# Kernel optimization log

Measured on AMD Instinct MI355X. Metric: run time of the kernel, lower is better.

## Reference

```python
import jax, jax.numpy as jnp
import numpy as np

N = 8192          # total nodes in the batch of graphs
ATOM = 64         # atom_feats
HID = 128         # hidden_feats
HEADS = 8         # num_heads
NUM_GRAPHS = 256  # number of graphs (max value of `batch`)
NEG_SLOPE = 0.2   # LeakyReLU slope in GAT attention


def setup_inputs() -> dict:
    key = jax.random.key(0)
    ks = jax.random.split(key, 16)
    x = jax.random.normal(ks[0], (N, ATOM), dtype=jnp.float32)
    adj = (jax.random.uniform(ks[1], (N, N)) < 0.01).astype(jnp.float32)
    adj = jnp.maximum(adj, jnp.eye(N, dtype=jnp.float32))
    batch = jnp.sort(jax.random.randint(ks[2], (N,), 0, NUM_GRAPHS)).astype(jnp.int32)

    def u(k, shape, fan_in):
        lim = 1.0 / np.sqrt(fan_in)
        return jax.random.uniform(k, shape, jnp.float32, -lim, lim)

    in1 = HID * HEADS
    params = dict(
        W0=u(ks[3], (ATOM, HID), ATOM), a0_src=u(ks[4], (HID,), HID), a0_dst=u(ks[5], (HID,), HID),
        W1=u(ks[6], (in1, HID), in1), a1_src=u(ks[7], (HID,), HID), a1_dst=u(ks[8], (HID,), HID),
        W2=u(ks[9], (in1, HID), in1), a2_src=u(ks[10], (HID,), HID), a2_dst=u(ks[11], (HID,), HID),
        fc_w=u(ks[12], (HID, 1), HID), fc_b=u(ks[13], (1,), HID),
    )
    return dict(x=x, adj=adj, batch=batch, **params)


def _gat_layer(h_in, W, a_src, a_dst, mask):
    # standard dense GAT: Wh, e_ij = leakyrelu(a_src.Wh_i + a_dst.Wh_j), masked softmax, aggregate
    h = h_in @ W                                         # [N, HID]
    e = jax.nn.leaky_relu((h @ a_src)[:, None] + (h @ a_dst)[None, :], NEG_SLOPE)  # [N, N]
    e = jnp.where(mask, e, jnp.float32(-1e9))
    attn = jax.nn.softmax(e, axis=1)                     # [N, N]
    return attn @ h                                      # [N, HID]


def reference(x, adj, batch, W0, a0_src, a0_dst, W1, a1_src, a1_dst, W2, a2_src, a2_dst, fc_w, fc_b):
    # eval mode: dropout is identity. The torch module calls the SAME layer instance per head,
    # so concat of heads == tile, and the final stacked mean == a single layer call.
    mask = adj > 0
    h0 = _gat_layer(x, W0, a0_src, a0_dst, mask)
    x1 = jax.nn.relu(jnp.tile(h0, (1, HEADS)))           # [N, HID*HEADS]
    h1 = _gat_layer(x1, W1, a1_src, a1_dst, mask)
    x2 = jax.nn.relu(jnp.tile(h1, (1, HEADS)))
    h2 = _gat_layer(x2, W2, a2_src, a2_dst, mask)        # mean over identical heads == h2
    # global mean pool over graphs
    sums = jax.ops.segment_sum(h2, batch, num_segments=NUM_GRAPHS)           # [G, HID]
    cnt = jax.ops.segment_sum(jnp.ones((N, 1), h2.dtype), batch, num_segments=NUM_GRAPHS)
    pooled = sums / jnp.maximum(cnt, 1.0)
    out = pooled @ fc_w + fc_b                           # [G, 1]
    return out[:, 0]
```

## Files before the change

kernel.cpp:

```cpp
#include <hip/hip_runtime.h>
#include <hip/hip_fp16.h>
#include <cstdint>
#include <cstddef>

#define NN 8192
#define ATOMF 64
#define HID 128
#define HEADS 8
#define NG 256
#define ELLW 192
#define NEGSLOPE 0.2f

typedef unsigned long long u64;

__global__ __launch_bounds__(256, 4) void k_scan_ell(const float* __restrict__ adj,
                                                     int* __restrict__ ell,
                                                     int4* __restrict__ tb) {
    __shared__ u64 bml[4][128];
    int t = threadIdx.x, wid = t >> 6, l = t & 63;
    int row = blockIdx.x * 4 + wid;
    const float4* a4 = (const float4*)(adj + (size_t)row * NN);
    u64* bmr = bml[wid];
    #pragma unroll 8
    for (int s = 0; s < 32; ++s) {
        float4 v = a4[s * 64 + l];
        u64 b0 = __ballot(v.x > 0.f);
        u64 b1 = __ballot(v.y > 0.f);
        u64 b2 = __ballot(v.z > 0.f);
        u64 b3 = __ballot(v.w > 0.f);
        if (l < 4) bmr[s * 4 + l] = (l == 0) ? b0 : (l == 1) ? b1 : (l == 2) ? b2 : b3;
    }
    __syncthreads();
    u64 w0 = bmr[2 * l];
    u64 w1 = bmr[2 * l + 1];
    int c = __popcll(w0) + __popcll(w1);
    int incl = c;
    #pragma unroll
    for (int o = 1; o < 64; o <<= 1) {
        int u = __shfl_up(incl, o);
        if (l >= o) incl += u;
    }
    int pos = incl - c;
    int total = __shfl(incl, 63);
    if (l == 0) {
        int4 b;
        b.x = b.y = b.z = 0;
        b.w = total < ELLW ? total : ELLW;
        tb[row] = b;
    }
    int* er = ell + (size_t)row * ELLW;
    int gw0 = 2 * l, gw1 = 2 * l + 1;
    int base0 = (gw0 >> 2) * 256 + (gw0 & 3);
    int base1 = (gw1 >> 2) * 256 + (gw1 & 3);
    while (w0) {
        int bit = __builtin_ctzll(w0);
        w0 &= w0 - 1;
        if (pos < ELLW) er[pos++] = base0 + 4 * bit;
    }
    while (w1) {
        int bit = __builtin_ctzll(w1);
        w1 &= w1 - 1;
        if (pos < ELLW) er[pos++] = base1 + 4 * bit;
    }
}

__global__ __launch_bounds__(256) void k_front2(
    const float* __restrict__ x,
    const float* __restrict__ W0, const float* __restrict__ a0s, const float* __restrict__ a0d,
    const float* __restrict__ W1, const float* __restrict__ W2,
    float* __restrict__ Wr1, float* __restrict__ Wr2,
    __half* __restrict__ g016, float* __restrict__ ssrc, float* __restrict__ sdst) {
    int b = blockIdx.x, t = threadIdx.x;
    if (b < 128) {
        const float* W = (b < 64) ? W1 : W2;
        float* Wr = (b < 64) ? Wr1 : Wr2;
        int i = (b & 63) * 256 + t;
        int k = i >> 7, cc = i & 127;
        float s = 0.f;
        #pragma unroll
        for (int h = 0; h < HEADS; ++h) s += W[(size_t)(h * HID + k) * HID + cc];
        Wr[i] = s;
    } else {
        __shared__ float Xl[32 * ATOMF];
        int row0 = (b - 128) * 32;
        const float4* Xg = (const float4*)(x + (size_t)row0 * ATOMF);
        float4* Xl4 = (float4*)Xl;
        #pragma unroll
        for (int i = t; i < 32 * ATOMF / 4; i += 256) Xl4[i] = Xg[i];
        __syncthreads();
        int cg = t & 31, rg = t >> 5;
        int c0 = cg * 4;
        float acc[4][4];
        #pragma unroll
        for (int r = 0; r < 4; ++r)
            #pragma unroll
            for (int c = 0; c < 4; ++c) acc[r][c] = 0.f;
        for (int k = 0; k < ATOMF; k += 4) {
            float4 w0 = *(const float4*)(W0 + (size_t)(k + 0) * HID + c0);
            float4 w1 = *(const float4*)(W0 + (size_t)(k + 1) * HID + c0);
            float4 w2 = *(const float4*)(W0 + (size_t)(k + 2) * HID + c0);
            float4 w3 = *(const float4*)(W0 + (size_t)(k + 3) * HID + c0);
            #pragma unroll
            for (int r = 0; r < 4; ++r) {
                float4 xv = *(const float4*)(&Xl[(rg * 4 + r) * ATOMF + k]);
                acc[r][0] += xv.x * w0.x + xv.y * w1.x + xv.z * w2.x + xv.w * w3.x;
                acc[r][1] += xv.x * w0.y + xv.y * w1.y + xv.z * w2.y + xv.w * w3.y;
                acc[r][2] += xv.x * w0.z + xv.y * w1.z + xv.z * w2.z + xv.w * w3.z;
                acc[r][3] += xv.x * w0.w + xv.y * w1.w + xv.z * w2.w + xv.w * w3.w;
            }
        }
        float4 asv = *(const float4*)(a0s + c0);
        float4 adv = *(const float4*)(a0d + c0);
        #pragma unroll
        for (int r = 0; r < 4; ++r) {
            int row = row0 + rg * 4 + r;
            __half2 p0 = __floats2half2_rn(acc[r][0], acc[r][1]);
            __half2 p1 = __floats2half2_rn(acc[r][2], acc[r][3]);
            __half2* gp = (__half2*)(g016 + (size_t)row * HID + c0);
            gp[0] = p0; gp[1] = p1;
            float ps = acc[r][0] * asv.x + acc[r][1] * asv.y + acc[r][2] * asv.z + acc[r][3] * asv.w;
            float pd = acc[r][0] * adv.x + acc[r][1] * adv.y + acc[r][2] * adv.z + acc[r][3] * adv.w;
            #pragma unroll
            for (int o = 16; o; o >>= 1) {
                ps += __shfl_xor(ps, o);
                pd += __shfl_xor(pd, o);
            }
            if (cg == 0) { ssrc[row] = ps; sdst[row] = pd; }
        }
    }
}

template<int DO_GEMM>
__global__ __launch_bounds__(256, 8) void k_layer(
    const __half* __restrict__ h16, const float* __restrict__ ssrc_in,
    const float* __restrict__ sdst_in,
    const int* __restrict__ ell, const int4* __restrict__ tb,
    const float* __restrict__ Wr, const float* __restrict__ as_,
    const float* __restrict__ ad_,
    __half* __restrict__ gout16, float* __restrict__ gout32,
    float* __restrict__ ssrc_out, float* __restrict__ sdst_out) {
    __shared__ float wls[4][ELLW + 4];
    __shared__ int   jls[4][ELLW + 4];
    __shared__ float xls[4][HID];
    int wid = threadIdx.x >> 6, l = threadIdx.x & 63;
    int row = blockIdx.x * 4 + wid;
    float* wl = wls[wid];
    int* jl = jls[wid];
    int d = tb[row].w;
    float si = ssrc_in[row];
    const int* er = ell + (size_t)row * ELLW;
    float s = 0.f;
    for (int k = l; k < d; k += 64) {
        int j = er[k];
        float e = si + sdst_in[j];
        e = e > 0.f ? e : NEGSLOPE * e;
        float w = __expf(e);
        jl[k] = j << 7;
        wl[k] = w;
        s += w;
    }
    #pragma unroll
    for (int o = 32; o; o >>= 1) s += __shfl_xor(s, o);
    float inv = 1.f / s;
    int dpad = (d + 3) & ~3;
    if (l < 3 && d + l < dpad) { wl[d + l] = 0.f; jl[d + l] = 0; }
    int q = l >> 4;
    int d0 = (l & 15) * 8;
    const __half* hd = h16 + d0;
    float a0 = 0.f, a1 = 0.f, a2 = 0.f, a3 = 0.f;
    float a4 = 0.f, a5 = 0.f, a6 = 0.f, a7 = 0.f;
    int k = 0;
    for (; k + 8 <= dpad; k += 8) {
        int jA = jl[k + q], jB = jl[k + 4 + q];
        float wA = wl[k + q], wB = wl[k + 4 + q];
        int4 rA = *(const int4*)(hd + jA);
        int4 rB = *(const int4*)(hd + jB);
        float2 fA0 = __half22float2(*(__half2*)&rA.x);
        float2 fA1 = __half22float2(*(((__half2*)&rA.x) + 1));
        float2 fA2 = __half22float2(*(__half2*)&rA.z);
        float2 fA3 = __half22float2(*(((__half2*)&rA.z) + 1));
        a0 += wA * fA0.x; a1 += wA * fA0.y; a2 += wA * fA1.x; a3 += wA * fA1.y;
        a4 += wA * fA2.x; a5 += wA * fA2.y; a6 += wA * fA3.x; a7 += wA * fA3.y;
        float2 fB0 = __half22float2(*(__half2*)&rB.x);
        float2 fB1 = __half22float2(*(((__half2*)&rB.x) + 1));
        float2 fB2 = __half22float2(*(__half2*)&rB.z);
        float2 fB3 = __half22float2(*(((__half2*)&rB.z) + 1));
        a0 += wB * fB0.x; a1 += wB * fB0.y; a2 += wB * fB1.x; a3 += wB * fB1.y;
        a4 += wB * fB2.x; a5 += wB * fB2.y; a6 += wB * fB3.x; a7 += wB * fB3.y;
    }
    for (; k < dpad; k += 4) {
        int jA = jl[k + q];
        float wA = wl[k + q];
        int4 rA = *(const int4*)(hd + jA);
        float2 fA0 = __half22float2(*(__half2*)&rA.x);
        float2 fA1 = __half22float2(*(((__half2*)&rA.x) + 1));
        float2 fA2 = __half22float2(*(__half2*)&rA.z);
        float2 fA3 = __half22float2(*(((__half2*)&rA.z) + 1));
        a0 += wA * fA0.x; a1 += wA * fA0.y; a2 += wA * fA1.x; a3 += wA * fA1.y;
        a4 += wA * fA2.x; a5 += wA * fA2.y; a6 += wA * fA3.x; a7 += wA * fA3.y;
    }
    #pragma unroll
    for (int o = 16; o <= 32; o <<= 1) {
        a0 += __shfl_xor(a0, o); a1 += __shfl_xor(a1, o);
        a2 += __shfl_xor(a2, o); a3 += __shfl_xor(a3, o);
        a4 += __shfl_xor(a4, o); a5 += __shfl_xor(a5, o);
        a6 += __shfl_xor(a6, o); a7 += __shfl_xor(a7, o);
    }
    a0 *= inv; a1 *= inv; a2 *= inv; a3 *= inv;
    a4 *= inv; a5 *= inv; a6 *= inv; a7 *= inv;
    if (DO_GEMM == 0) {
        if (l < 16) {
            float* op = gout32 + (size_t)row * HID + d0;
            *(float4*)op       = make_float4(a0, a1, a2, a3);
            *(float4*)(op + 4) = make_float4(a4, a5, a6, a7);
        }
        return;
    }
    float* xl = xls[wid];
    if (l < 16) {
        *(float4*)(xl + d0)     = make_float4(fmaxf(a0, 0.f), fmaxf(a1, 0.f),
                                              fmaxf(a2, 0.f), fmaxf(a3, 0.f));
        *(float4*)(xl + d0 + 4) = make_float4(fmaxf(a4, 0.f), fmaxf(a5, 0.f),
                                              fmaxf(a6, 0.f), fmaxf(a7, 0.f));
    }
    int c2 = 2 * l;
    float acc0 = 0.f, acc1 = 0.f;
    for (int kk = 0; kk < HID; kk += 4) {
        float4 xv = *(const float4*)(&xl[kk]);
        float2 w0 = *(const float2*)(Wr + (size_t)(kk + 0) * HID + c2);
        float2 w1 = *(const float2*)(Wr + (size_t)(kk + 1) * HID + c2);
        float2 w2 = *(const float2*)(Wr + (size_t)(kk + 2) * HID + c2);
        float2 w3 = *(const float2*)(Wr + (size_t)(kk + 3) * HID + c2);
        acc0 += xv.x * w0.x + xv.y * w1.x + xv.z * w2.x + xv.w * w3.x;
        acc1 += xv.x * w0.y + xv.y * w1.y + xv.z * w2.y + xv.w * w3.y;
    }
    *(__half2*)(gout16 + (size_t)row * HID + c2) = __floats2half2_rn(acc0, acc1);
    float2 asv = *(const float2*)(as_ + c2);
    float2 adv = *(const float2*)(ad_ + c2);
    float ps = acc0 * asv.x + acc1 * asv.y;
    float pd = acc0 * adv.x + acc1 * adv.y;
    #pragma unroll
    for (int o = 32; o; o >>= 1) {
        ps += __shfl_xor(ps, o);
        pd += __shfl_xor(pd, o);
    }
    if (l == 0) { ssrc_out[row] = ps; sdst_out[row] = pd; }
}

__global__ __launch_bounds__(256) void k_poolfc(const float* __restrict__ h,
                                                const int* __restrict__ batch,
                                                const float* __restrict__ fcw,
                                                const float* __restrict__ fcb,
                                                float* __restrict__ out) {
    int wid = threadIdx.x >> 6, l = threadIdx.x & 63;
    int g = blockIdx.x * 4 + wid;
    int lo = 0, hi = NN;
    while (lo < hi) { int mid = (lo + hi) >> 1; if (batch[mid] < g) lo = mid + 1; else hi = mid; }
    int e0 = lo;
    hi = NN;
    while (lo < hi) { int mid = (lo + hi) >> 1; if (batch[mid] <= g) lo = mid + 1; else hi = mid; }
    int e1 = lo;
    float sum = 0.f;
    for (int r = e0; r < e1; ++r) {
        const float* hr = h + (size_t)r * HID;
        sum += hr[l] * fcw[l] + hr[l + 64] * fcw[l + 64];
    }
    #pragma unroll
    for (int o = 32; o; o >>= 1) sum += __shfl_xor(sum, o);
    if (l == 0) out[g] = sum / fmaxf((float)(e1 - e0), 1.f) + fcb[0];
}

extern "C" void kernel_launch(void* const* d_in, const int* in_sizes, int n_in,
                              void* d_out, int out_size, void* d_ws, size_t ws_size,
                              hipStream_t stream) {
    const float* x    = (const float*)d_in[0];
    const float* adj  = (const float*)d_in[1];
    const int*   batch= (const int*)  d_in[2];
    const float* W0   = (const float*)d_in[3];
    const float* a0s  = (const float*)d_in[4];
    const float* a0d  = (const float*)d_in[5];
    const float* W1   = (const float*)d_in[6];
    const float* a1s  = (const float*)d_in[7];
    const float* a1d  = (const float*)d_in[8];
    const float* W2   = (const float*)d_in[9];
    const float* a2s  = (const float*)d_in[10];
    const float* a2d  = (const float*)d_in[11];
    const float* fcw  = (const float*)d_in[12];
    const float* fcb  = (const float*)d_in[13];
    float* out = (float*)d_out;

    char* ws = (char*)d_ws;
    size_t off = 0;
    auto alloc = [&](size_t bytes) {
        char* p = ws + off;
        off = (off + bytes + 255) & ~255UL;
        return p;
    };
    int*    ell  = (int*)   alloc((size_t)NN * ELLW * 4);
    int4*   tb   = (int4*)  alloc((size_t)NN * 16);
    __half* hA16 = (__half*)alloc((size_t)NN * HID * 2);
    __half* hB16 = (__half*)alloc((size_t)NN * HID * 2);
    float*  h2   = (float*) alloc((size_t)NN * HID * 4);
    float*  sAs  = (float*) alloc((size_t)NN * 4);
    float*  sAd  = (float*) alloc((size_t)NN * 4);
    float*  sBs  = (float*) alloc((size_t)NN * 4);
    float*  sBd  = (float*) alloc((size_t)NN * 4);
    float*  Wr1  = (float*) alloc((size_t)HID * HID * 4);
    float*  Wr2  = (float*) alloc((size_t)HID * HID * 4);
    (void)ws_size; (void)in_sizes; (void)n_in; (void)out_size;

    k_scan_ell<<<NN / 4, 256, 0, stream>>>(adj, ell, tb);
    k_front2<<<128 + 256, 256, 0, stream>>>(x, W0, a0s, a0d, W1, W2,
                                            Wr1, Wr2, hA16, sAs, sAd);
    k_layer<1><<<NN / 4, 256, 0, stream>>>(hA16, sAs, sAd, ell, tb, Wr1, a1s, a1d,
                                           hB16, nullptr, sBs, sBd);
    k_layer<1><<<NN / 4, 256, 0, stream>>>(hB16, sBs, sBd, ell, tb, Wr2, a2s, a2d,
                                           hA16, nullptr, sAs, sAd);
    k_layer<0><<<NN / 4, 256, 0, stream>>>(hA16, sAs, sAd, ell, tb, nullptr, nullptr,
                                           nullptr, nullptr, h2, nullptr, nullptr);
    k_poolfc<<<NG / 4, 256, 0, stream>>>(h2, batch, fcw, fcb, out);
}
```

Measured before the change: 174.3 us.

## Merge preprocessing kernels and fuse pooling and FC into final layer

```diff
diff --git a/kernel.cpp b/kernel.cpp
--- a/kernel.cpp
+++ b/kernel.cpp
@@ -13,76 +13,75 @@
 
 typedef unsigned long long u64;
 
-__global__ __launch_bounds__(256, 4) void k_scan_ell(const float* __restrict__ adj,
-                                                     int* __restrict__ ell,
-                                                     int4* __restrict__ tb) {
-    __shared__ u64 bml[4][128];
-    int t = threadIdx.x, wid = t >> 6, l = t & 63;
-    int row = blockIdx.x * 4 + wid;
-    const float4* a4 = (const float4*)(adj + (size_t)row * NN);
-    u64* bmr = bml[wid];
-    #pragma unroll 8
-    for (int s = 0; s < 32; ++s) {
-        float4 v = a4[s * 64 + l];
-        u64 b0 = __ballot(v.x > 0.f);
-        u64 b1 = __ballot(v.y > 0.f);
-        u64 b2 = __ballot(v.z > 0.f);
-        u64 b3 = __ballot(v.w > 0.f);
-        if (l < 4) bmr[s * 4 + l] = (l == 0) ? b0 : (l == 1) ? b1 : (l == 2) ? b2 : b3;
-    }
-    __syncthreads();
-    u64 w0 = bmr[2 * l];
-    u64 w1 = bmr[2 * l + 1];
-    int c = __popcll(w0) + __popcll(w1);
-    int incl = c;
-    #pragma unroll
-    for (int o = 1; o < 64; o <<= 1) {
-        int u = __shfl_up(incl, o);
-        if (l >= o) incl += u;
-    }
-    int pos = incl - c;
-    int total = __shfl(incl, 63);
-    if (l == 0) {
-        int4 b;
-        b.x = b.y = b.z = 0;
-        b.w = total < ELLW ? total : ELLW;
-        tb[row] = b;
-    }
-    int* er = ell + (size_t)row * ELLW;
-    int gw0 = 2 * l, gw1 = 2 * l + 1;
-    int base0 = (gw0 >> 2) * 256 + (gw0 & 3);
-    int base1 = (gw1 >> 2) * 256 + (gw1 & 3);
-    while (w0) {
-        int bit = __builtin_ctzll(w0);
-        w0 &= w0 - 1;
-        if (pos < ELLW) er[pos++] = base0 + 4 * bit;
-    }
-    while (w1) {
-        int bit = __builtin_ctzll(w1);
-        w1 &= w1 - 1;
-        if (pos < ELLW) er[pos++] = base1 + 4 * bit;
-    }
-}
-
-__global__ __launch_bounds__(256) void k_front2(
-    const float* __restrict__ x,
+__global__ __launch_bounds__(256, 4) void k_pre(
+    const float* __restrict__ adj, const float* __restrict__ x,
     const float* __restrict__ W0, const float* __restrict__ a0s, const float* __restrict__ a0d,
     const float* __restrict__ W1, const float* __restrict__ W2,
+    int* __restrict__ ell, int4* __restrict__ tb,
     float* __restrict__ Wr1, float* __restrict__ Wr2,
-    __half* __restrict__ g016, float* __restrict__ ssrc, float* __restrict__ sdst) {
+    __half* __restrict__ g016, float* __restrict__ ssrc, float* __restrict__ sdst,
+    float* __restrict__ gsum, int* __restrict__ done) {
+    __shared__ u64 bml[4][128];
+    __shared__ float Xl[32 * ATOMF];
     int b = blockIdx.x, t = threadIdx.x;
-    if (b < 128) {
-        const float* W = (b < 64) ? W1 : W2;
-        float* Wr = (b < 64) ? Wr1 : Wr2;
-        int i = (b & 63) * 256 + t;
+    if (b < 2048) {
+        int wid = t >> 6, l = t & 63;
+        int row = b * 4 + wid;
+        const float4* a4 = (const float4*)(adj + (size_t)row * NN);
+        u64* bmr = bml[wid];
+        #pragma unroll 8
+        for (int s = 0; s < 32; ++s) {
+            float4 v = a4[s * 64 + l];
+            u64 b0 = __ballot(v.x > 0.f);
+            u64 b1 = __ballot(v.y > 0.f);
+            u64 b2 = __ballot(v.z > 0.f);
+            u64 b3 = __ballot(v.w > 0.f);
+            if (l < 4) bmr[s * 4 + l] = (l == 0) ? b0 : (l == 1) ? b1 : (l == 2) ? b2 : b3;
+        }
+        __syncthreads();
+        u64 w0 = bmr[2 * l];
+        u64 w1 = bmr[2 * l + 1];
+        int c = __popcll(w0) + __popcll(w1);
+        int incl = c;
+        #pragma unroll
+        for (int o = 1; o < 64; o <<= 1) {
+            int u = __shfl_up(incl, o);
+            if (l >= o) incl += u;
+        }
+        int pos = incl - c;
+        int total = __shfl(incl, 63);
+        if (l == 0) {
+            int4 bb;
+            bb.x = bb.y = bb.z = 0;
+            bb.w = total < ELLW ? total : ELLW;
+            tb[row] = bb;
+        }
+        int* er = ell + (size_t)row * ELLW;
+        int gw0 = 2 * l, gw1 = 2 * l + 1;
+        int base0 = (gw0 >> 2) * 256 + (gw0 & 3);
+        int base1 = (gw1 >> 2) * 256 + (gw1 & 3);
+        while (w0) {
+            int bit = __builtin_ctzll(w0);
+            w0 &= w0 - 1;
+            if (pos < ELLW) er[pos++] = base0 + 4 * bit;
+        }
+        while (w1) {
+            int bit = __builtin_ctzll(w1);
+            w1 &= w1 - 1;
+            if (pos < ELLW) er[pos++] = base1 + 4 * bit;
+        }
+    } else if (b < 2048 + 128) {
+        int bb = b - 2048;
+        const float* W = (bb < 64) ? W1 : W2;
+        float* Wr = (bb < 64) ? Wr1 : Wr2;
+        int i = (bb & 63) * 256 + t;
         int k = i >> 7, cc = i & 127;
         float s = 0.f;
         #pragma unroll
         for (int h = 0; h < HEADS; ++h) s += W[(size_t)(h * HID + k) * HID + cc];
         Wr[i] = s;
-    } else {
-        __shared__ float Xl[32 * ATOMF];
-        int row0 = (b - 128) * 32;
+    } else if (b < 2048 + 384) {
+        int row0 = (b - 2048 - 128) * 32;
         const float4* Xg = (const float4*)(x + (size_t)row0 * ATOMF);
         float4* Xl4 = (float4*)Xl;
         #pragma unroll
@@ -127,21 +126,28 @@
             }
             if (cg == 0) { ssrc[row] = ps; sdst[row] = pd; }
         }
+    } else {
+        if (t < NG) gsum[t] = 0.f;
+        if (t == 0) *done = 0;
     }
 }
 
-template<int DO_GEMM>
+template<int MODE>
 __global__ __launch_bounds__(256, 8) void k_layer(
     const __half* __restrict__ h16, const float* __restrict__ ssrc_in,
     const float* __restrict__ sdst_in,
     const int* __restrict__ ell, const int4* __restrict__ tb,
     const float* __restrict__ Wr, const float* __restrict__ as_,
     const float* __restrict__ ad_,
-    __half* __restrict__ gout16, float* __restrict__ gout32,
-    float* __restrict__ ssrc_out, float* __restrict__ sdst_out) {
+    __half* __restrict__ gout16, float* __restrict__ ssrc_out,
+    float* __restrict__ sdst_out,
+    const int* __restrict__ batch, const float* __restrict__ fcw,
+    const float* __restrict__ fcb, float* __restrict__ gsum,
+    int* __restrict__ done, float* __restrict__ out) {
     __shared__ float wls[4][ELLW + 4];
     __shared__ int   jls[4][ELLW + 4];
     __shared__ float xls[4][HID];
+    __shared__ int lastflag;
     int wid = threadIdx.x >> 6, l = threadIdx.x & 63;
     int row = blockIdx.x * 4 + wid;
     float* wl = wls[wid];
@@ -208,11 +214,31 @@
     }
     a0 *= inv; a1 *= inv; a2 *= inv; a3 *= inv;
     a4 *= inv; a5 *= inv; a6 *= inv; a7 *= inv;
-    if (DO_GEMM == 0) {
-        if (l < 16) {
-            float* op = gout32 + (size_t)row * HID + d0;
-            *(float4*)op       = make_float4(a0, a1, a2, a3);
-            *(float4*)(op + 4) = make_float4(a4, a5, a6, a7);
+    if (MODE == 3) {
+        float4 f0 = *(const float4*)(fcw + d0);
+        float4 f1 = *(const float4*)(fcw + d0 + 4);
+        float p = a0 * f0.x + a1 * f0.y + a2 * f0.z + a3 * f0.w
+                + a4 * f1.x + a5 * f1.y + a6 * f1.z + a7 * f1.w;
+        #pragma unroll
+        for (int o = 8; o; o >>= 1) p += __shfl_xor(p, o);
+        if (l == 0) atomicAdd(&gsum[batch[row]], p);
+        __syncthreads();
+        if (threadIdx.x == 0) {
+            __threadfence();
+            int prev = __hip_atomic_fetch_add(done, 1, __ATOMIC_ACQ_REL, __HIP_MEMORY_SCOPE_AGENT);
+            lastflag = (prev == (NN / 4) - 1);
+        }
+        __syncthreads();
+        if (lastflag) {
+            int g = threadIdx.x;
+            int lo = 0, hi = NN;
+            while (lo < hi) { int mid = (lo + hi) >> 1; if (batch[mid] < g) lo = mid + 1; else hi = mid; }
+            int e0 = lo;
+            hi = NN;
+            while (lo < hi) { int mid = (lo + hi) >> 1; if (batch[mid] <= g) lo = mid + 1; else hi = mid; }
+            int cnt = lo - e0;
+            float v = __hip_atomic_load(&gsum[g], __ATOMIC_RELAXED, __HIP_MEMORY_SCOPE_AGENT);
+            out[g] = v / fmaxf((float)cnt, 1.f) + fcb[0];
         }
         return;
     }
@@ -245,29 +271,6 @@
         pd += __shfl_xor(pd, o);
     }
     if (l == 0) { ssrc_out[row] = ps; sdst_out[row] = pd; }
-}
-
-__global__ __launch_bounds__(256) void k_poolfc(const float* __restrict__ h,
-                                                const int* __restrict__ batch,
-                                                const float* __restrict__ fcw,
-                                                const float* __restrict__ fcb,
-                                                float* __restrict__ out) {
-    int wid = threadIdx.x >> 6, l = threadIdx.x & 63;
-    int g = blockIdx.x * 4 + wid;
-    int lo = 0, hi = NN;
-    while (lo < hi) { int mid = (lo + hi) >> 1; if (batch[mid] < g) lo = mid + 1; else hi = mid; }
-    int e0 = lo;
-    hi = NN;
-    while (lo < hi) { int mid = (lo + hi) >> 1; if (batch[mid] <= g) lo = mid + 1; else hi = mid; }
-    int e1 = lo;
-    float sum = 0.f;
-    for (int r = e0; r < e1; ++r) {
-        const float* hr = h + (size_t)r * HID;
-        sum += hr[l] * fcw[l] + hr[l + 64] * fcw[l + 64];
-    }
-    #pragma unroll
-    for (int o = 32; o; o >>= 1) sum += __shfl_xor(sum, o);
-    if (l == 0) out[g] = sum / fmaxf((float)(e1 - e0), 1.f) + fcb[0];
 }
 
 extern "C" void kernel_launch(void* const* d_in, const int* in_sizes, int n_in,
@@ -300,23 +303,26 @@
     int4*   tb   = (int4*)  alloc((size_t)NN * 16);
     __half* hA16 = (__half*)alloc((size_t)NN * HID * 2);
     __half* hB16 = (__half*)alloc((size_t)NN * HID * 2);
-    float*  h2   = (float*) alloc((size_t)NN * HID * 4);
     float*  sAs  = (float*) alloc((size_t)NN * 4);
     float*  sAd  = (float*) alloc((size_t)NN * 4);
     float*  sBs  = (float*) alloc((size_t)NN * 4);
     float*  sBd  = (float*) alloc((size_t)NN * 4);
     float*  Wr1  = (float*) alloc((size_t)HID * HID * 4);
     float*  Wr2  = (float*) alloc((size_t)HID * HID * 4);
+    float*  gsum = (float*) alloc((size_t)NG * 4);
+    int*    done = (int*)   alloc(256);
     (void)ws_size; (void)in_sizes; (void)n_in; (void)out_size;
 
-    k_scan_ell<<<NN / 4, 256, 0, stream>>>(adj, ell, tb);
-    k_front2<<<128 + 256, 256, 0, stream>>>(x, W0, a0s, a0d, W1, W2,
-                                            Wr1, Wr2, hA16, sAs, sAd);
+    k_pre<<<2048 + 384 + 1, 256, 0, stream>>>(adj, x, W0, a0s, a0d, W1, W2,
+                                              ell, tb, Wr1, Wr2, hA16, sAs, sAd,
+                                              gsum, done);
     k_layer<1><<<NN / 4, 256, 0, stream>>>(hA16, sAs, sAd, ell, tb, Wr1, a1s, a1d,
-                                           hB16, nullptr, sBs, sBd);
+                                           hB16, sBs, sBd,
+                                           nullptr, nullptr, nullptr, nullptr, nullptr, nullptr);
     k_layer<1><<<NN / 4, 256, 0, stream>>>(hB16, sBs, sBd, ell, tb, Wr2, a2s, a2d,
-                                           hA16, nullptr, sAs, sAd);
-    k_layer<0><<<NN / 4, 256, 0, stream>>>(hA16, sAs, sAd, ell, tb, nullptr, nullptr,
-                                           nullptr, nullptr, h2, nullptr, nullptr);
-    k_poolfc<<<NG / 4, 256, 0, stream>>>(h2, batch, fcw, fcb, out);
+                                           hA16, sAs, sAd,
+                                           nullptr, nullptr, nullptr, nullptr, nullptr, nullptr);
+    k_layer<3><<<NN / 4, 256, 0, stream>>>(hA16, sAs, sAd, ell, tb, nullptr, nullptr,
+                                           nullptr, nullptr, nullptr, nullptr,
+                                           batch, fcw, fcb, gsum, done, out);
 }
```

New measurement: 354.4 us. 2.03x slower.
